# Kernel optimization log

Hardware: AMD Instinct MI355X
Metric: run time of the kernel (lower is better)

## Reference

```python
import jax, jax.numpy as jnp
import numpy as np

N_NODES = 200000
N_EDGES = 600000
IN_CH = 128
OUT_CH = 128
E_DIM = 16


def _linear_params(key, fan_in, fan_out):
    kw, kb = jax.random.split(key)
    s = 1.0 / np.sqrt(fan_in)
    W = jax.random.uniform(kw, (fan_in, fan_out), jnp.float32, -s, s)
    b = jax.random.uniform(kb, (fan_out,), jnp.float32, -s, s)
    return W, b


def setup_inputs() -> dict:
    key = jax.random.key(0)
    ks = jax.random.split(key, 12)
    x = jax.random.normal(ks[0], (N_NODES, IN_CH), jnp.float32)
    edge_index = jax.random.randint(ks[1], (2, N_EDGES), 0, N_NODES, jnp.int64)
    edge_attr = jax.random.normal(ks[2], (N_EDGES, E_DIM), jnp.float32)
    W_enc, b_enc = _linear_params(ks[3], IN_CH, OUT_CH)
    # conv1: edge lin (e_dim->out) + 2-layer MLP, trainable eps (init 0)
    We1, be1 = _linear_params(ks[4], E_DIM, OUT_CH)
    W11, b11 = _linear_params(ks[5], OUT_CH, OUT_CH)
    W12, b12 = _linear_params(ks[6], OUT_CH, OUT_CH)
    eps1 = jnp.zeros((), jnp.float32)
    # conv2
    We2, be2 = _linear_params(ks[7], E_DIM, OUT_CH)
    W21, b21 = _linear_params(ks[8], OUT_CH, OUT_CH)
    W22, b22 = _linear_params(ks[9], OUT_CH, OUT_CH)
    eps2 = jnp.zeros((), jnp.float32)
    return {"x": x, "edge_index": edge_index, "edge_attr": edge_attr,
            "W_enc": W_enc, "b_enc": b_enc,
            "We1": We1, "be1": be1, "W11": W11, "b11": b11, "W12": W12, "b12": b12, "eps1": eps1,
            "We2": We2, "be2": be2, "W21": W21, "b21": b21, "W22": W22, "b22": b22, "eps2": eps2}


def _gine_conv(h, src, dst, edge_feat, eps, W1, b1, W2, b2):
    # message: ReLU(x_j + lin_edge(edge_attr)); aggregate: scatter-sum to dst
    msg = jax.nn.relu(h[src] + edge_feat)          # [E, C]
    agg = jax.ops.segment_sum(msg, dst, num_segments=h.shape[0])  # [N, C]
    z = (1.0 + eps) * h + agg
    z = jax.nn.relu(z @ W1 + b1)
    return jax.nn.relu(z @ W2 + b2)


def reference(x, edge_index, edge_attr,
              W_enc, b_enc,
              We1, be1, W11, b11, W12, b12, eps1,
              We2, be2, W21, b21, W22, b22, eps2):
    src, dst = edge_index[0], edge_index[1]
    h = jax.nn.relu(x @ W_enc + b_enc)
    ef1 = edge_attr @ We1 + be1
    h = jax.nn.relu(_gine_conv(h, src, dst, ef1, eps1, W11, b11, W12, b12))
    # dropout (p=0.2) is identity in eval mode
    ef2 = edge_attr @ We2 + be2
    out = jax.nn.relu(_gine_conv(h, src, dst, ef2, eps2, W21, b21, W22, b22))
    return out
```

## Files before the change

### kernel.cpp

```cpp
#include <hip/hip_runtime.h>
#include <stdint.h>

#define N_NODES 200000
#define N_EDGES 600000
#define SCAN_CHUNK 1024
#define SCAN_BLOCKS ((N_NODES + SCAN_CHUNK - 1) / SCAN_CHUNK)

typedef __attribute__((ext_vector_type(8))) short short8;
typedef __attribute__((ext_vector_type(4))) float floatx4;
typedef __attribute__((ext_vector_type(2))) float floatx2;

static __device__ __forceinline__ unsigned short f2bf(float f) {
  union { float f; unsigned u; } c; c.f = f;
  unsigned u = c.u;
  unsigned r = (u + 0x7fffu + ((u >> 16) & 1u)) >> 16;
  return (unsigned short)r;
}
static __device__ __forceinline__ float asf(unsigned u) {
  union { unsigned u; float f; } c; c.u = u; return c.f;
}

__global__ __launch_bounds__(256) void prep_kernel(
    const float* w0, const float* w1, const float* w2, const float* w3, const float* w4,
    unsigned short* out) {
  const float* src;
  switch (blockIdx.y) {
    case 0: src = w0; break;
    case 1: src = w1; break;
    case 2: src = w2; break;
    case 3: src = w3; break;
    default: src = w4; break;
  }
  unsigned short* dst = out + (size_t)blockIdx.y * 16384;
  int t = blockIdx.x * 256 + threadIdx.x;
#pragma unroll
  for (int i = 0; i < 4; ++i) {
    int idx = t + 4096 * i;
    int n = idx >> 7, k = idx & 127;
    dst[idx] = f2bf(src[k * 128 + n]);
  }
}

__global__ __launch_bounds__(256) void hist_kernel(const int* __restrict__ dst, int* deg, int E) {
  int e = blockIdx.x * 256 + threadIdx.x;
  if (e < E) atomicAdd(&deg[dst[e]], 1);
}

__global__ __launch_bounds__(256) void scan_sum_kernel(const int* __restrict__ deg, int* partial,
                                                       int n) {
  __shared__ int wsum[4];
  const int tid = threadIdx.x, lane = tid & 63, wid = tid >> 6;
  int idx0 = blockIdx.x * SCAN_CHUNK + tid * 4;
  int s = 0;
#pragma unroll
  for (int j = 0; j < 4; ++j) {
    int ix = idx0 + j;
    if (ix < n) s += deg[ix];
  }
#pragma unroll
  for (int d = 32; d >= 1; d >>= 1) s += __shfl_down(s, d, 64);
  if (lane == 0) wsum[wid] = s;
  __syncthreads();
  if (tid == 0) partial[blockIdx.x] = wsum[0] + wsum[1] + wsum[2] + wsum[3];
}

__global__ __launch_bounds__(256) void scan_partials_kernel(int* partial, int* off, int nb, int n) {
  __shared__ int wsum[4];
  const int tid = threadIdx.x, lane = tid & 63, wid = tid >> 6;
  int val = (tid < nb) ? partial[tid] : 0;
  int incl = val;
#pragma unroll
  for (int d = 1; d < 64; d <<= 1) {
    int t = __shfl_up(incl, d, 64);
    if (lane >= d) incl += t;
  }
  if (lane == 63) wsum[wid] = incl;
  __syncthreads();
  int base = 0;
  for (int w = 0; w < wid; ++w) base += wsum[w];
  int excl = base + incl - val;
  if (tid < nb) partial[tid] = excl;
  if (tid == 0) off[n] = wsum[0] + wsum[1] + wsum[2] + wsum[3];
}

__global__ __launch_bounds__(256) void scan_apply_kernel(const int* __restrict__ partial, int* off,
                                                         int* cursor, int n) {
  __shared__ int wsum[4];
  const int tid = threadIdx.x, lane = tid & 63, wid = tid >> 6;
  int idx0 = blockIdx.x * SCAN_CHUNK + tid * 4;
  int v[4];
  int s = 0;
#pragma unroll
  for (int j = 0; j < 4; ++j) {
    int ix = idx0 + j;
    v[j] = (ix < n) ? off[ix] : 0;
    s += v[j];
  }
  int incl = s;
#pragma unroll
  for (int d = 1; d < 64; d <<= 1) {
    int t = __shfl_up(incl, d, 64);
    if (lane >= d) incl += t;
  }
  if (lane == 63) wsum[wid] = incl;
  __syncthreads();
  int base = partial[blockIdx.x];
  for (int w = 0; w < wid; ++w) base += wsum[w];
  int running = base + incl - s;
#pragma unroll
  for (int j = 0; j < 4; ++j) {
    int ix = idx0 + j;
    if (ix < n) { off[ix] = running; cursor[ix] = running; }
    running += v[j];
  }
}

__global__ __launch_bounds__(256) void scatter_kernel(const int* __restrict__ dst,
                                                      const int* __restrict__ src, int* cursor,
                                                      int* eids, int* srcs, int E) {
  int e = blockIdx.x * 256 + threadIdx.x;
  if (e < E) {
    int p = atomicAdd(&cursor[dst[e]], 1);
    eids[p] = e;
    srcs[p] = src[e];
  }
}

__global__ __launch_bounds__(256) void agg_z_kernel(
    const unsigned short* __restrict__ hB, const int* __restrict__ off,
    const int* __restrict__ eids, const int* __restrict__ srcs,
    const float* __restrict__ edge_attr,
    const float* __restrict__ We, const float* __restrict__ be,
    const float* __restrict__ epsPtr, unsigned short* __restrict__ z) {
  const int lane = threadIdx.x & 63;
  const int wv = threadIdx.x >> 6;
  const int c = lane * 2;
  floatx2 wr[16];
#pragma unroll
  for (int d = 0; d < 16; ++d) {
    float2 t = *((const float2*)(We + d * 128 + c));
    wr[d].x = t.x; wr[d].y = t.y;
  }
  const float2 bev = *((const float2*)(be + c));
  const float epsp = 1.0f + epsPtr[0];
  const int waveId = blockIdx.x * 4 + wv;
  const int nWaves = gridDim.x * 4;
  for (int node = waveId; node < N_NODES; node += nWaves) {
    floatx2 acc; acc.x = 0.0f; acc.y = 0.0f;
    const int s0 = off[node], s1 = off[node + 1];
    for (int base = s0; base < s1; base += 64) {
      int nrem = s1 - base; if (nrem > 64) nrem = 64;
      int e_l = 0, sn_l = 0;
      if (base + lane < s1) {
        e_l = eids[base + lane];
        sn_l = srcs[base + lane];
      }
      for (int j = 0; j < nrem; ++j) {
        const int e = __builtin_amdgcn_readlane(e_l, j);
        const int sn = __builtin_amdgcn_readlane(sn_l, j);
        const unsigned hw = *((const unsigned*)(hB + (size_t)sn * 128 + c));
        const float4 q0 = *((const float4*)(edge_attr + (size_t)e * 16));
        const float4 q1 = *((const float4*)(edge_attr + (size_t)e * 16 + 4));
        const float4 q2 = *((const float4*)(edge_attr + (size_t)e * 16 + 8));
        const float4 q3 = *((const float4*)(edge_attr + (size_t)e * 16 + 12));
        floatx2 ef; ef.x = bev.x; ef.y = bev.y;
        ef += q0.x * wr[0];
        ef += q0.y * wr[1];
        ef += q0.z * wr[2];
        ef += q0.w * wr[3];
        ef += q1.x * wr[4];
        ef += q1.y * wr[5];
        ef += q1.z * wr[6];
        ef += q1.w * wr[7];
        ef += q2.x * wr[8];
        ef += q2.y * wr[9];
        ef += q2.z * wr[10];
        ef += q2.w * wr[11];
        ef += q3.x * wr[12];
        ef += q3.y * wr[13];
        ef += q3.z * wr[14];
        ef += q3.w * wr[15];
        floatx2 hv;
        hv.x = asf(hw << 16);
        hv.y = asf(hw & 0xffff0000u);
        floatx2 m = ef + hv;
        m.x = fmaxf(m.x, 0.0f);
        m.y = fmaxf(m.y, 0.0f);
        acc += m;
      }
    }
    const unsigned hw = *((const unsigned*)(hB + (size_t)node * 128 + c));
    const float hx = asf(hw << 16);
    const float hy = asf(hw & 0xffff0000u);
    unsigned p = (unsigned)f2bf(fmaf(epsp, hx, acc.x)) |
                 ((unsigned)f2bf(fmaf(epsp, hy, acc.y)) << 16);
    *((unsigned*)(z + (size_t)node * 128 + c)) = p;
  }
}

__global__ __launch_bounds__(256) void mlp_kernel(
    const void* __restrict__ Ain, int aIsBf16,
    const unsigned short* __restrict__ W1t, const float* __restrict__ b1,
    const unsigned short* __restrict__ W2t, const float* __restrict__ b2,
    int twoStage, int outBf16, void* __restrict__ out) {
  __shared__ unsigned short sA[64][136];
  __shared__ unsigned short sW[128][136];
  const int tid = threadIdx.x;
  const int lane = tid & 63;
  const int wv = tid >> 6;
  const int lr = lane & 15, quad = lane >> 4;
  const int mw = wv >> 1, nw = wv & 1;
  const size_t rowBase = (size_t)blockIdx.x * 64;

  if (aIsBf16) {
    const uint4* src = (const uint4*)((const unsigned short*)Ain + rowBase * 128);
#pragma unroll
    for (int i = 0; i < 4; ++i) {
      int idx = tid + 256 * i;
      int r = idx >> 4, c8 = idx & 15;
      uint4 v = src[idx];
      *((uint4*)&sA[r][c8 * 8]) = v;
    }
  } else {
    const float4* src = (const float4*)((const float*)Ain + rowBase * 128);
#pragma unroll
    for (int i = 0; i < 8; ++i) {
      int idx = tid + 256 * i;
      int r = idx >> 5, c4 = idx & 31;
      float4 v = src[idx];
      uint2 p;
      p.x = (unsigned)f2bf(v.x) | ((unsigned)f2bf(v.y) << 16);
      p.y = (unsigned)f2bf(v.z) | ((unsigned)f2bf(v.w) << 16);
      *((uint2*)&sA[r][c4 * 4]) = p;
    }
  }
  {
    const uint4* srcw = (const uint4*)W1t;
#pragma unroll
    for (int i = 0; i < 8; ++i) {
      int idx = tid + 256 * i;
      int r = idx >> 4, c8 = idx & 15;
      *((uint4*)&sW[r][c8 * 8]) = srcw[idx];
    }
  }
  __syncthreads();

  floatx4 acc[2][4];
#pragma unroll
  for (int mi = 0; mi < 2; ++mi)
#pragma unroll
    for (int ni = 0; ni < 4; ++ni)
#pragma unroll
      for (int i = 0; i < 4; ++i) acc[mi][ni][i] = 0.0f;

#pragma unroll
  for (int kk = 0; kk < 4; ++kk) {
    short8 a[2], b[4];
#pragma unroll
    for (int mi = 0; mi < 2; ++mi)
      a[mi] = *((const short8*)&sA[32 * mw + 16 * mi + lr][kk * 32 + quad * 8]);
#pragma unroll
    for (int ni = 0; ni < 4; ++ni)
      b[ni] = *((const short8*)&sW[64 * nw + 16 * ni + lr][kk * 32 + quad * 8]);
#pragma unroll
    for (int mi = 0; mi < 2; ++mi)
#pragma unroll
      for (int ni = 0; ni < 4; ++ni)
        acc[mi][ni] = __builtin_amdgcn_mfma_f32_16x16x32_bf16(a[mi], b[ni], acc[mi][ni], 0, 0, 0);
  }

  if (!twoStage) {
#pragma unroll
    for (int mi = 0; mi < 2; ++mi)
#pragma unroll
      for (int ni = 0; ni < 4; ++ni)
#pragma unroll
        for (int i = 0; i < 4; ++i) {
          int row = 32 * mw + 16 * mi + quad * 4 + i;
          int col = 64 * nw + 16 * ni + lr;
          float v = fmaxf(acc[mi][ni][i] + b1[col], 0.0f);
          if (outBf16)
            ((unsigned short*)out)[(rowBase + row) * 128 + col] = f2bf(v);
          else
            ((float*)out)[(rowBase + row) * 128 + col] = v;
        }
    return;
  }

  __syncthreads();
#pragma unroll
  for (int mi = 0; mi < 2; ++mi)
#pragma unroll
    for (int ni = 0; ni < 4; ++ni)
#pragma unroll
      for (int i = 0; i < 4; ++i) {
        int row = 32 * mw + 16 * mi + quad * 4 + i;
        int col = 64 * nw + 16 * ni + lr;
        sA[row][col] = f2bf(fmaxf(acc[mi][ni][i] + b1[col], 0.0f));
      }
  {
    const uint4* srcw = (const uint4*)W2t;
#pragma unroll
    for (int i = 0; i < 8; ++i) {
      int idx = tid + 256 * i;
      int r = idx >> 4, c8 = idx & 15;
      *((uint4*)&sW[r][c8 * 8]) = srcw[idx];
    }
  }
  __syncthreads();

  floatx4 acc2[2][4];
#pragma unroll
  for (int mi = 0; mi < 2; ++mi)
#pragma unroll
    for (int ni = 0; ni < 4; ++ni)
#pragma unroll
      for (int i = 0; i < 4; ++i) acc2[mi][ni][i] = 0.0f;

#pragma unroll
  for (int kk = 0; kk < 4; ++kk) {
    short8 a[2], b[4];
#pragma unroll
    for (int mi = 0; mi < 2; ++mi)
      a[mi] = *((const short8*)&sA[32 * mw + 16 * mi + lr][kk * 32 + quad * 8]);
#pragma unroll
    for (int ni = 0; ni < 4; ++ni)
      b[ni] = *((const short8*)&sW[64 * nw + 16 * ni + lr][kk * 32 + quad * 8]);
#pragma unroll
    for (int mi = 0; mi < 2; ++mi)
#pragma unroll
      for (int ni = 0; ni < 4; ++ni)
        acc2[mi][ni] = __builtin_amdgcn_mfma_f32_16x16x32_bf16(a[mi], b[ni], acc2[mi][ni], 0, 0, 0);
  }

#pragma unroll
  for (int mi = 0; mi < 2; ++mi)
#pragma unroll
    for (int ni = 0; ni < 4; ++ni)
#pragma unroll
      for (int i = 0; i < 4; ++i) {
        int row = 32 * mw + 16 * mi + quad * 4 + i;
        int col = 64 * nw + 16 * ni + lr;
        float v = fmaxf(acc2[mi][ni][i] + b2[col], 0.0f);
        if (outBf16)
          ((unsigned short*)out)[(rowBase + row) * 128 + col] = f2bf(v);
        else
          ((float*)out)[(rowBase + row) * 128 + col] = v;
      }
}

extern "C" void kernel_launch(void* const* d_in, const int* in_sizes, int n_in,
                              void* d_out, int out_size, void* d_ws, size_t ws_size,
                              hipStream_t stream) {
  (void)in_sizes; (void)n_in; (void)out_size; (void)ws_size;
  const float* x = (const float*)d_in[0];
  const int* eidx = (const int*)d_in[1];
  const int* esrc = eidx;
  const int* edst = eidx + N_EDGES;
  const float* eattr = (const float*)d_in[2];
  const float* W_enc = (const float*)d_in[3];
  const float* b_enc = (const float*)d_in[4];
  const float* We1 = (const float*)d_in[5];
  const float* be1 = (const float*)d_in[6];
  const float* W11 = (const float*)d_in[7];
  const float* b11 = (const float*)d_in[8];
  const float* W12 = (const float*)d_in[9];
  const float* b12 = (const float*)d_in[10];
  const float* eps1 = (const float*)d_in[11];
  const float* We2 = (const float*)d_in[12];
  const float* be2 = (const float*)d_in[13];
  const float* W21 = (const float*)d_in[14];
  const float* b21 = (const float*)d_in[15];
  const float* W22 = (const float*)d_in[16];
  const float* b22 = (const float*)d_in[17];
  const float* eps2 = (const float*)d_in[18];

  char* ws = (char*)d_ws;
  unsigned short* wt = (unsigned short*)ws;
  unsigned short* hB = (unsigned short*)(ws + 163840);
  unsigned short* bufZ = (unsigned short*)(ws + 163840 + 51200000ull);
  int* off = (int*)(ws + 163840 + 2ull * 51200000ull);
  int* cursor = off + (N_NODES + 1);
  int* eids = cursor + N_NODES;
  int* srcs = eids + N_EDGES;
  int* partial = srcs + N_EDGES;

  unsigned short* Wt_enc = wt;
  unsigned short* Wt11 = wt + 16384;
  unsigned short* Wt12 = wt + 2 * 16384;
  unsigned short* Wt21 = wt + 3 * 16384;
  unsigned short* Wt22 = wt + 4 * 16384;

  hipMemsetAsync(off, 0, (N_NODES + 1) * sizeof(int), stream);
  prep_kernel<<<dim3(16, 5), 256, 0, stream>>>(W_enc, W11, W12, W21, W22, wt);

  mlp_kernel<<<3125, 256, 0, stream>>>(x, 0, Wt_enc, b_enc, Wt_enc, b_enc, 0, 1, hB);

  hist_kernel<<<(N_EDGES + 255) / 256, 256, 0, stream>>>(edst, off, N_EDGES);
  scan_sum_kernel<<<SCAN_BLOCKS, 256, 0, stream>>>(off, partial, N_NODES);
  scan_partials_kernel<<<1, 256, 0, stream>>>(partial, off, SCAN_BLOCKS, N_NODES);
  scan_apply_kernel<<<SCAN_BLOCKS, 256, 0, stream>>>(partial, off, cursor, N_NODES);
  scatter_kernel<<<(N_EDGES + 255) / 256, 256, 0, stream>>>(edst, esrc, cursor, eids, srcs,
                                                            N_EDGES);

  agg_z_kernel<<<4096, 256, 0, stream>>>(hB, off, eids, srcs, eattr, We1, be1, eps1, bufZ);
  mlp_kernel<<<3125, 256, 0, stream>>>(bufZ, 1, Wt11, b11, Wt12, b12, 1, 1, hB);
  agg_z_kernel<<<4096, 256, 0, stream>>>(hB, off, eids, srcs, eattr, We2, be2, eps2, bufZ);
  mlp_kernel<<<3125, 256, 0, stream>>>(bufZ, 1, Wt21, b21, Wt22, b22, 1, 0, d_out);
}
```

Measured before the change: 563.0 us.

## Permute edge attributes into CSR order and edge-balance aggregation across waves

The scatter pass now copies each edge's 16 attributes into dst-sorted order, so aggregation reads them contiguously instead of gathering through an edge-id indirection. A new partition kernel binary-searches the CSR offsets so each wave gets a contiguous node range with roughly equal edge counts. The aggregation loop also batches up to four neighbor row loads before computing, to raise memory-level parallelism. This costs an extra 38 MB workspace buffer and an extra write pass in scatter, and waves may get uneven node counts.

```diff
diff --git a/kernel.cpp b/kernel.cpp
--- a/kernel.cpp
+++ b/kernel.cpp
@@ -5,6 +5,8 @@
 #define N_EDGES 600000
 #define SCAN_CHUNK 1024
 #define SCAN_BLOCKS ((N_NODES + SCAN_CHUNK - 1) / SCAN_CHUNK)
+#define GRID_AGG 4096
+#define NWAVES (GRID_AGG * 4)
 
 typedef __attribute__((ext_vector_type(8))) short short8;
 typedef __attribute__((ext_vector_type(4))) float floatx4;
@@ -116,20 +118,37 @@
 }
 
 __global__ __launch_bounds__(256) void scatter_kernel(const int* __restrict__ dst,
-                                                      const int* __restrict__ src, int* cursor,
-                                                      int* eids, int* srcs, int E) {
+                                                      const int* __restrict__ src,
+                                                      const float* __restrict__ eattr, int* cursor,
+                                                      int* srcs, float* eaC, int E) {
   int e = blockIdx.x * 256 + threadIdx.x;
   if (e < E) {
     int p = atomicAdd(&cursor[dst[e]], 1);
-    eids[p] = e;
     srcs[p] = src[e];
-  }
+    const float4* q = (const float4*)(eattr + (size_t)e * 16);
+    float4* o = (float4*)(eaC + (size_t)p * 16);
+    o[0] = q[0]; o[1] = q[1]; o[2] = q[2]; o[3] = q[3];
+  }
+}
+
+__global__ __launch_bounds__(256) void partition_kernel(const int* __restrict__ off,
+                                                        int* waveStart) {
+  int w = blockIdx.x * 256 + threadIdx.x;
+  if (w > NWAVES) return;
+  if (w == NWAVES) { waveStart[w] = N_NODES; return; }
+  long long t = (long long)w * N_EDGES / NWAVES;
+  int lo = 0, hi = N_NODES;
+  while (lo < hi) {
+    int mid = (lo + hi) >> 1;
+    if (off[mid] < (int)t) lo = mid + 1; else hi = mid;
+  }
+  waveStart[w] = lo;
 }
 
 __global__ __launch_bounds__(256) void agg_z_kernel(
     const unsigned short* __restrict__ hB, const int* __restrict__ off,
-    const int* __restrict__ eids, const int* __restrict__ srcs,
-    const float* __restrict__ edge_attr,
+    const int* __restrict__ waveStart, const int* __restrict__ srcs,
+    const float* __restrict__ eaC,
     const float* __restrict__ We, const float* __restrict__ be,
     const float* __restrict__ epsPtr, unsigned short* __restrict__ z) {
   const int lane = threadIdx.x & 63;
@@ -143,59 +162,82 @@
   }
   const float2 bev = *((const float2*)(be + c));
   const float epsp = 1.0f + epsPtr[0];
-  const int waveId = blockIdx.x * 4 + wv;
-  const int nWaves = gridDim.x * 4;
-  for (int node = waveId; node < N_NODES; node += nWaves) {
+  const int w = blockIdx.x * 4 + wv;
+  const int n0 = waveStart[w];
+  const int n1 = waveStart[w + 1];
+  if (n0 >= n1) return;
+
+  int obase = n0;
+  {
+    int ix = obase + lane; if (ix > n1) ix = n1;
+  }
+  int ix0 = obase + lane; if (ix0 > n1) ix0 = n1;
+  int offv = off[ix0];
+  int ii = __builtin_amdgcn_readlane(offv, 0);
+  int ebase = ii;
+  int sx0 = ebase + lane; if (sx0 > N_EDGES - 1) sx0 = N_EDGES - 1;
+  int sbuf = srcs[sx0];
+
+#define EDGE_COMPUTE(EIDX, HW) { \
+    const float* ea = eaC + (size_t)(EIDX) * 16; \
+    const float4 q0 = *((const float4*)(ea)); \
+    const float4 q1 = *((const float4*)(ea + 4)); \
+    const float4 q2 = *((const float4*)(ea + 8)); \
+    const float4 q3 = *((const float4*)(ea + 12)); \
+    floatx2 efa; efa.x = bev.x; efa.y = bev.y; \
+    floatx2 efb; efb.x = 0.0f; efb.y = 0.0f; \
+    efa += q0.x * wr[0]; efb += q0.y * wr[1]; \
+    efa += q0.z * wr[2]; efb += q0.w * wr[3]; \
+    efa += q1.x * wr[4]; efb += q1.y * wr[5]; \
+    efa += q1.z * wr[6]; efb += q1.w * wr[7]; \
+    efa += q2.x * wr[8]; efb += q2.y * wr[9]; \
+    efa += q2.z * wr[10]; efb += q2.w * wr[11]; \
+    efa += q3.x * wr[12]; efb += q3.y * wr[13]; \
+    efa += q3.z * wr[14]; efb += q3.w * wr[15]; \
+    floatx2 hv; hv.x = asf((HW) << 16); hv.y = asf((HW) & 0xffff0000u); \
+    floatx2 mm = (efa + efb) + hv; \
+    mm.x = fmaxf(mm.x, 0.0f); mm.y = fmaxf(mm.y, 0.0f); \
+    acc += mm; }
+
+  for (int n = n0; n < n1; ++n) {
+    if (n + 1 - obase >= 64) {
+      obase = n;
+      int ix = obase + lane; if (ix > n1) ix = n1;
+      offv = off[ix];
+    }
+    const int eE = __builtin_amdgcn_readlane(offv, n + 1 - obase);
+    const unsigned hwn = *((const unsigned*)(hB + (size_t)n * 128 + c));
     floatx2 acc; acc.x = 0.0f; acc.y = 0.0f;
-    const int s0 = off[node], s1 = off[node + 1];
-    for (int base = s0; base < s1; base += 64) {
-      int nrem = s1 - base; if (nrem > 64) nrem = 64;
-      int e_l = 0, sn_l = 0;
-      if (base + lane < s1) {
-        e_l = eids[base + lane];
-        sn_l = srcs[base + lane];
+    while (ii < eE) {
+      int m = eE - ii; if (m > 4) m = 4;
+      if (ii + m > ebase + 64) {
+        ebase = ii;
+        int sx = ebase + lane; if (sx > N_EDGES - 1) sx = N_EDGES - 1;
+        sbuf = srcs[sx];
       }
-      for (int j = 0; j < nrem; ++j) {
-        const int e = __builtin_amdgcn_readlane(e_l, j);
-        const int sn = __builtin_amdgcn_readlane(sn_l, j);
-        const unsigned hw = *((const unsigned*)(hB + (size_t)sn * 128 + c));
-        const float4 q0 = *((const float4*)(edge_attr + (size_t)e * 16));
-        const float4 q1 = *((const float4*)(edge_attr + (size_t)e * 16 + 4));
-        const float4 q2 = *((const float4*)(edge_attr + (size_t)e * 16 + 8));
-        const float4 q3 = *((const float4*)(edge_attr + (size_t)e * 16 + 12));
-        floatx2 ef; ef.x = bev.x; ef.y = bev.y;
-        ef += q0.x * wr[0];
-        ef += q0.y * wr[1];
-        ef += q0.z * wr[2];
-        ef += q0.w * wr[3];
-        ef += q1.x * wr[4];
-        ef += q1.y * wr[5];
-        ef += q1.z * wr[6];
-        ef += q1.w * wr[7];
-        ef += q2.x * wr[8];
-        ef += q2.y * wr[9];
-        ef += q2.z * wr[10];
-        ef += q2.w * wr[11];
-        ef += q3.x * wr[12];
-        ef += q3.y * wr[13];
-        ef += q3.z * wr[14];
-        ef += q3.w * wr[15];
-        floatx2 hv;
-        hv.x = asf(hw << 16);
-        hv.y = asf(hw & 0xffff0000u);
-        floatx2 m = ef + hv;
-        m.x = fmaxf(m.x, 0.0f);
-        m.y = fmaxf(m.y, 0.0f);
-        acc += m;
-      }
-    }
-    const unsigned hw = *((const unsigned*)(hB + (size_t)node * 128 + c));
-    const float hx = asf(hw << 16);
-    const float hy = asf(hw & 0xffff0000u);
+      const int j = ii - ebase;
+      const int sn0 = __builtin_amdgcn_readlane(sbuf, j);
+      const int sn1_ = __builtin_amdgcn_readlane(sbuf, (j + 1) & 63);
+      const int sn2_ = __builtin_amdgcn_readlane(sbuf, (j + 2) & 63);
+      const int sn3_ = __builtin_amdgcn_readlane(sbuf, (j + 3) & 63);
+      unsigned hw0, hw1 = 0, hw2 = 0, hw3 = 0;
+      hw0 = *((const unsigned*)(hB + (size_t)sn0 * 128 + c));
+      if (m > 1) hw1 = *((const unsigned*)(hB + (size_t)sn1_ * 128 + c));
+      if (m > 2) hw2 = *((const unsigned*)(hB + (size_t)sn2_ * 128 + c));
+      if (m > 3) hw3 = *((const unsigned*)(hB + (size_t)sn3_ * 128 + c));
+      EDGE_COMPUTE(ii, hw0);
+      if (m > 1) EDGE_COMPUTE(ii + 1, hw1);
+      if (m > 2) EDGE_COMPUTE(ii + 2, hw2);
+      if (m > 3) EDGE_COMPUTE(ii + 3, hw3);
+      ii += m;
+    }
+    const float hx = asf(hwn << 16);
+    const float hy = asf(hwn & 0xffff0000u);
     unsigned p = (unsigned)f2bf(fmaf(epsp, hx, acc.x)) |
                  ((unsigned)f2bf(fmaf(epsp, hy, acc.y)) << 16);
-    *((unsigned*)(z + (size_t)node * 128 + c)) = p;
-  }
+    *((unsigned*)(z + (size_t)n * 128 + c)) = p;
+  }
+#undef EDGE_COMPUTE
 }
 
 __global__ __launch_bounds__(256) void mlp_kernel(
@@ -376,14 +418,16 @@
   const float* eps2 = (const float*)d_in[18];
 
   char* ws = (char*)d_ws;
-  unsigned short* wt = (unsigned short*)ws;
-  unsigned short* hB = (unsigned short*)(ws + 163840);
-  unsigned short* bufZ = (unsigned short*)(ws + 163840 + 51200000ull);
-  int* off = (int*)(ws + 163840 + 2ull * 51200000ull);
-  int* cursor = off + (N_NODES + 1);
-  int* eids = cursor + N_NODES;
-  int* srcs = eids + N_EDGES;
-  int* partial = srcs + N_EDGES;
+  size_t o = 0;
+  unsigned short* wt = (unsigned short*)(ws + o); o += 163840;
+  unsigned short* hB = (unsigned short*)(ws + o); o += 51200000ull;
+  unsigned short* bufZ = (unsigned short*)(ws + o); o += 51200000ull;
+  float* eaC = (float*)(ws + o); o += 38400000ull;
+  int* off = (int*)(ws + o); o += ((N_NODES + 1) * 4 + 15) / 16 * 16;
+  int* cursor = (int*)(ws + o); o += ((size_t)N_NODES * 4 + 15) / 16 * 16;
+  int* srcs = (int*)(ws + o); o += (size_t)N_EDGES * 4;
+  int* partial = (int*)(ws + o); o += (SCAN_BLOCKS * 4 + 15) / 16 * 16;
+  int* waveStart = (int*)(ws + o); o += (size_t)(NWAVES + 1) * 4;
 
   unsigned short* Wt_enc = wt;
   unsigned short* Wt11 = wt + 16384;
@@ -400,11 +444,12 @@
   scan_sum_kernel<<<SCAN_BLOCKS, 256, 0, stream>>>(off, partial, N_NODES);
   scan_partials_kernel<<<1, 256, 0, stream>>>(partial, off, SCAN_BLOCKS, N_NODES);
   scan_apply_kernel<<<SCAN_BLOCKS, 256, 0, stream>>>(partial, off, cursor, N_NODES);
-  scatter_kernel<<<(N_EDGES + 255) / 256, 256, 0, stream>>>(edst, esrc, cursor, eids, srcs,
+  partition_kernel<<<(NWAVES + 256) / 256, 256, 0, stream>>>(off, waveStart);
+  scatter_kernel<<<(N_EDGES + 255) / 256, 256, 0, stream>>>(edst, esrc, eattr, cursor, srcs, eaC,
                                                             N_EDGES);
 
-  agg_z_kernel<<<4096, 256, 0, stream>>>(hB, off, eids, srcs, eattr, We1, be1, eps1, bufZ);
+  agg_z_kernel<<<GRID_AGG, 256, 0, stream>>>(hB, off, waveStart, srcs, eaC, We1, be1, eps1, bufZ);
   mlp_kernel<<<3125, 256, 0, stream>>>(bufZ, 1, Wt11, b11, Wt12, b12, 1, 1, hB);
-  agg_z_kernel<<<4096, 256, 0, stream>>>(hB, off, eids, srcs, eattr, We2, be2, eps2, bufZ);
+  agg_z_kernel<<<GRID_AGG, 256, 0, stream>>>(hB, off, waveStart, srcs, eaC, We2, be2, eps2, bufZ);
   mlp_kernel<<<3125, 256, 0, stream>>>(bufZ, 1, Wt21, b21, Wt22, b22, 1, 0, d_out);
 }
```

Measured after the change: 516.6 us. -8.2%, faster.
